# Kernel tuning notes

Measured on AMD Instinct MI355X. Metric: run time of the kernel, lower is better.

## Reference

```python
import jax, jax.numpy as jnp
import numpy as np
import math

L = 6; D = 768; NH = 12; DH = D // NH; V = 2048; CTX = 512; B = 16; T = 512
PAD_ID = 0; PAD_X = 18; PAD_Y = 32; N_ACTIONS = 9


def _layernorm(x, s, b, eps=1e-5):
    m = jnp.mean(x, axis=-1, keepdims=True)
    v = jnp.mean((x - m) ** 2, axis=-1, keepdims=True)
    return (x - m) * jax.lax.rsqrt(v + eps) * s + b


def setup_inputs() -> dict:
    key = jax.random.key(0)
    ks = jax.random.split(key, 16)
    s = 0.02
    x_emb = jax.random.normal(ks[4], (19, D), jnp.float32) * s
    x_emb = x_emb.at[PAD_X].set(0.0)  # padding_idx row is zero in torch
    y_emb = jax.random.normal(ks[5], (33, D), jnp.float32) * s
    y_emb = y_emb.at[PAD_Y].set(0.0)
    return {
        "history_cards": jax.random.randint(ks[0], (B, T), 0, V),
        "history_players": jax.random.randint(ks[1], (B, T), 0, 2),
        "deck": jax.random.randint(ks[2], (B, 8), 0, V),
        "opp_deck": jax.random.randint(ks[3], (B, 8), 0, V),
        "tok_emb": jax.random.normal(ks[6], (V, D), jnp.float32) * s,
        "player_emb": jax.random.normal(ks[7], (2, D), jnp.float32) * s,
        "pos_emb": jax.random.normal(ks[8], (CTX, D), jnp.float32) * s,
        "x_emb": x_emb,
        "y_emb": y_emb,
        "ln1_s": jnp.ones((L, D), jnp.float32),
        "ln1_b": jnp.zeros((L, D), jnp.float32),
        "qkv_w": jax.random.normal(ks[9], (L, D, 3 * D), jnp.float32) * s,
        "qkv_b": jnp.zeros((L, 3 * D), jnp.float32),
        "proj_w": jax.random.normal(ks[10], (L, D, D), jnp.float32) * s,
        "proj_b": jnp.zeros((L, D), jnp.float32),
        "ln2_s": jnp.ones((L, D), jnp.float32),
        "ln2_b": jnp.zeros((L, D), jnp.float32),
        "fc1_w": jax.random.normal(ks[11], (L, D, 4 * D), jnp.float32) * s,
        "fc1_b": jnp.zeros((L, 4 * D), jnp.float32),
        "fc2_w": jax.random.normal(ks[12], (L, 4 * D, D), jnp.float32) * s,
        "fc2_b": jnp.zeros((L, D), jnp.float32),
        "lnf_s": jnp.ones((D,), jnp.float32),
        "lnf_b": jnp.zeros((D,), jnp.float32),
        "head_w": jax.random.normal(ks[13], (D, N_ACTIONS), jnp.float32) * s,
        "head_b": jnp.zeros((N_ACTIONS,), jnp.float32),
    }


def reference(history_cards, history_players, deck, opp_deck,
              tok_emb, player_emb, pos_emb, x_emb, y_emb,
              ln1_s, ln1_b, qkv_w, qkv_b, proj_w, proj_b,
              ln2_s, ln2_b, fc1_w, fc1_b, fc2_w, fc2_b,
              lnf_s, lnf_b, head_w, head_b):
    Bc, Tc = history_cards.shape
    attn_mask = history_cards != PAD_ID                      # (B,T) True = valid
    all_pad = ~jnp.any(attn_mask, axis=1)
    attn_mask = attn_mask.at[:, 0].set(attn_mask[:, 0] | all_pad)

    # multi-embedding sum (history_x/history_y are None => padding rows = 0)
    h = (tok_emb[history_cards]
         + player_emb[jnp.clip(history_players, 0, 1)]
         + x_emb[PAD_X] + y_emb[PAD_Y]
         + jnp.mean(tok_emb[deck], axis=1, keepdims=True)
         + jnp.mean(tok_emb[opp_deck], axis=1, keepdims=True))
    x = h + pos_emb[:Tc][None]                               # (B,T,D)

    causal = jnp.tril(jnp.ones((Tc, Tc), bool))
    mask = causal[None, None, :, :] & attn_mask[:, None, None, :]  # (B,1,T,T)
    neg_inf = jnp.float32(-jnp.inf)
    scale = 1.0 / math.sqrt(DH)

    for i in range(L):
        # attention
        xn = _layernorm(x, ln1_s[i], ln1_b[i])
        qkv = xn @ qkv_w[i] + qkv_b[i]
        q, k, v = jnp.split(qkv, 3, axis=-1)
        q = q.reshape(Bc, Tc, NH, DH)
        k = k.reshape(Bc, Tc, NH, DH)
        v = v.reshape(Bc, Tc, NH, DH)
        scores = jnp.einsum('bihd,bjhd->bhij', q, k) * scale
        scores = jnp.where(mask, scores, neg_inf)
        w = jax.nn.softmax(scores, axis=-1)
        w = jnp.nan_to_num(w, nan=0.0, posinf=0.0, neginf=0.0)
        y = jnp.einsum('bhij,bjhd->bihd', w, v).reshape(Bc, Tc, D)
        x = x + (y @ proj_w[i] + proj_b[i])
        # MLP
        xn = _layernorm(x, ln2_s[i], ln2_b[i])
        hmid = jax.nn.gelu(xn @ fc1_w[i] + fc1_b[i], approximate=False)
        x = x + (hmid @ fc2_w[i] + fc2_b[i])

    x = _layernorm(x, lnf_s, lnf_b)
    last_idx = jnp.clip(jnp.sum(attn_mask.astype(jnp.int32), axis=1) - 1, 0, None)
    last_h = x[jnp.arange(Bc), last_idx]                     # (B,D)
    return last_h @ head_w + head_b                          # (B,9)
```

## Files before the change

### kernel.cpp

```cpp
#include <hip/hip_runtime.h>
#include <hip/hip_bf16.h>
#include <math.h>

typedef __hip_bfloat16 bf16;
typedef __bf16 bf16x8 __attribute__((ext_vector_type(8)));
typedef float f32x4 __attribute__((ext_vector_type(4)));

__device__ __forceinline__ float b2f(bf16 v){ return __bfloat162float(v); }
__device__ __forceinline__ bf16  f2b(float v){ return __float2bfloat16(v); }

__device__ __forceinline__ float gelu_f(float v){
    float y = v * (1.f + 0.044715f * v * v);
    return v / (1.f + __expf(-1.5957691216057308f * y));
}

__device__ __forceinline__ void gl_lds16(const bf16* g, bf16* l) {
    __builtin_amdgcn_global_load_lds((const __attribute__((address_space(1))) unsigned int*)g,
                                     (__attribute__((address_space(3))) unsigned int*)l, 16, 0, 0);
}

__device__ __forceinline__ uint2 pack4bf(const float* v){
    union { unsigned short e[4]; uint2 u; } pk;
    #pragma unroll
    for (int r = 0; r < 4; r++) pk.e[r] = __builtin_bit_cast(unsigned short, f2b(v[r]));
    return pk.u;
}

__device__ __forceinline__ void phase_bar() {
    __builtin_amdgcn_sched_barrier(0);
    __builtin_amdgcn_s_barrier();
    __builtin_amdgcn_sched_barrier(0);
}

__device__ __forceinline__ void supertile_map(int bid, int ntc, int& mt, int& nt) {
    const int slot = bid >> 3, xcd = bid & 7;
    const int g = 4 * ntc;
    const int chunk = slot / g;
    const int r = slot - chunk * g;
    const int ml = r / ntc;
    mt = xcd * 4 + ml;
    nt = chunk * ntc + (r - ml * ntc);
}

__global__ __launch_bounds__(256) void deckmean_k(const int* __restrict__ deck, const int* __restrict__ opp,
                                                  const float* __restrict__ tok, float* __restrict__ deckm)
{
    int b = blockIdx.x, w = blockIdx.y;
    const int* dk = (w ? opp : deck) + b * 8;
    int idx[8];
    #pragma unroll
    for (int j = 0; j < 8; j++) idx[j] = dk[j];
    float* out = deckm + (size_t)(w * 16 + b) * 768;
    for (int d = threadIdx.x; d < 768; d += 256) {
        float s = 0.f;
        #pragma unroll
        for (int j = 0; j < 8; j++) s += tok[(size_t)idx[j] * 768 + d];
        out[d] = s * 0.125f;
    }
}

__global__ __launch_bounds__(512) void mask_k(const int* __restrict__ cards, int* __restrict__ maskb,
                                              int* __restrict__ lastidx)
{
    int b = blockIdx.x, t = threadIdx.x;
    int m = (cards[b * 512 + t] != 0) ? 1 : 0;
    maskb[b * 512 + t] = m;
    __shared__ int red[512];
    red[t] = m; __syncthreads();
    for (int st = 256; st > 0; st >>= 1) { if (t < st) red[t] += red[t + st]; __syncthreads(); }
    if (t == 0) {
        int cnt = red[0];
        if (cnt == 0) { maskb[b * 512] = 1; cnt = 1; }
        lastidx[b] = cnt - 1;
    }
}

__global__ __launch_bounds__(256) void embed_k(const int* __restrict__ cards, const int* __restrict__ players,
                                               const float* __restrict__ tok, const float* __restrict__ pemb,
                                               const float* __restrict__ pos, const float* __restrict__ deckm,
                                               float* __restrict__ x)
{
    int t = blockIdx.x;
    int b = t >> 9, ti = t & 511;
    int cd = cards[t];
    int p = players[t]; p = p < 0 ? 0 : (p > 1 ? 1 : p);
    const float* tr  = tok  + (size_t)cd * 768;
    const float* pr  = pemb + (size_t)p  * 768;
    const float* po  = pos  + (size_t)ti * 768;
    const float* dm = deckm + (size_t)b * 768;
    const float* om = deckm + (size_t)(16 + b) * 768;
    float* xr = x + (size_t)t * 768;
    for (int d = threadIdx.x; d < 768; d += 256)
        xr[d] = tr[d] + pr[d] + po[d] + dm[d] + om[d];
}

__global__ __launch_bounds__(192) void ln_k(const float* __restrict__ x, const float* __restrict__ s,
                                            const float* __restrict__ b, bf16* __restrict__ out)
{
    int row = blockIdx.x, tid = threadIdx.x;
    float4 v = ((const float4*)(x + (size_t)row * 768))[tid];
    float sum = v.x + v.y + v.z + v.w;
    float sq  = v.x * v.x + v.y * v.y + v.z * v.z + v.w * v.w;
    #pragma unroll
    for (int off = 32; off > 0; off >>= 1) {
        sum += __shfl_xor(sum, off, 64);
        sq  += __shfl_xor(sq,  off, 64);
    }
    __shared__ float red[6];
    int wv = tid >> 6;
    if ((tid & 63) == 0) { red[wv] = sum; red[3 + wv] = sq; }
    __syncthreads();
    float S = red[0] + red[1] + red[2];
    float Q = red[3] + red[4] + red[5];
    float mean = S * (1.f / 768.f);
    float var  = Q * (1.f / 768.f) - mean * mean;
    float rstd = rsqrtf(var + 1e-5f);
    float4 sv = ((const float4*)s)[tid];
    float4 bv = ((const float4*)b)[tid];
    float o[4] = { (v.x - mean) * rstd * sv.x + bv.x, (v.y - mean) * rstd * sv.y + bv.y,
                   (v.z - mean) * rstd * sv.z + bv.z, (v.w - mean) * rstd * sv.w + bv.w };
    ((uint2*)(out + (size_t)row * 768))[tid] = pack4bf(o);
}

__global__ __launch_bounds__(256) void transpose4_k(const float* __restrict__ qw, const float* __restrict__ pw,
                                                    const float* __restrict__ f1, const float* __restrict__ f2,
                                                    bf16* __restrict__ oq, bf16* __restrict__ op,
                                                    bf16* __restrict__ o1, bf16* __restrict__ o2)
{
    int t = blockIdx.x;
    const float* in; bf16* out; int K, N, nbx;
    if (t < 432)       { in = qw; out = oq; K = 768;  N = 2304; nbx = 36; }
    else if (t < 576)  { in = pw; out = op; K = 768;  N = 768;  t -= 432;  nbx = 12; }
    else if (t < 1152) { in = f1; out = o1; K = 768;  N = 3072; t -= 576;  nbx = 48; }
    else               { in = f2; out = o2; K = 3072; N = 768;  t -= 1152; nbx = 12; }
    int n0 = (t % nbx) * 64, k0 = (t / nbx) * 64;
    int kq = threadIdx.x & 15, nq = threadIdx.x >> 4;
    float4 rr[4];
    #pragma unroll
    for (int r = 0; r < 4; r++)
        rr[r] = *(const float4*)&in[(size_t)(k0 + kq * 4 + r) * N + n0 + nq * 4];
    const float* fp = (const float*)rr;
    #pragma unroll
    for (int c = 0; c < 4; c++) {
        float v[4] = { fp[c], fp[4 + c], fp[8 + c], fp[12 + c] };
        *(uint2*)&out[(size_t)(n0 + nq * 4 + c) * K + k0 + kq * 4] = pack4bf(v);
    }
}

__global__ __launch_bounds__(512, 2) void gemmn128b_k(const bf16* __restrict__ A, const bf16* __restrict__ BT,
                                                      const float* __restrict__ bias, bf16* __restrict__ out,
                                                      int N, int K, int act, int ntc)
{
    __shared__ __align__(16) bf16 MA0[256 * 64];
    __shared__ __align__(16) bf16 MA1[256 * 64];
    __shared__ __align__(16) bf16 MA2[256 * 64];
    __shared__ __align__(16) bf16 MB0[128 * 64];
    __shared__ __align__(16) bf16 MB1[128 * 64];
    __shared__ __align__(16) bf16 MB2[128 * 64];

    const int tid  = threadIdx.x;
    const int lane = tid & 63, wid = tid >> 6;
    const int quad = lane >> 4, l16 = lane & 15;
    const int wr = wid >> 1, wc = wid & 1;
    const int cg0 = quad ^ (l16 & 7);
    const int cg1 = cg0 ^ 4;

    int mt, nt;
    supertile_map((int)blockIdx.x, ntc, mt, nt);
    const int m0 = mt * 256, n0 = nt * 128;

    const int srow = wid * 8 + (lane >> 3);
    const int scg  = (lane & 7) ^ (lane >> 3);
    const bf16* sa[4]; const bf16* sb[2];
    #pragma unroll
    for (int s = 0; s < 4; s++) sa[s] = A  + (size_t)(m0 + s * 64 + srow) * K + scg * 8;
    #pragma unroll
    for (int s = 0; s < 2; s++) sb[s] = BT + (size_t)(n0 + s * 64 + srow) * K + scg * 8;

#define MSTG6(NA, NB) { \
    gl_lds16(sa[0], &NA[(0 * 64 + wid * 8) * 64]); gl_lds16(sa[1], &NA[(1 * 64 + wid * 8) * 64]); \
    gl_lds16(sa[2], &NA[(2 * 64 + wid * 8) * 64]); gl_lds16(sa[3], &NA[(3 * 64 + wid * 8) * 64]); \
    gl_lds16(sb[0], &NB[(0 * 64 + wid * 8) * 64]); gl_lds16(sb[1], &NB[(1 * 64 + wid * 8) * 64]); }
#define MADV { _Pragma("unroll") for (int s = 0; s < 4; s++) sa[s] += 64; sb[0] += 64; sb[1] += 64; }
#define MLD(cg, NA, NB) { _Pragma("unroll") for (int i = 0; i < 4; i++) { \
    bfv[i] = __builtin_bit_cast(bf16x8, *(const uint4*)&NB[(wc * 64 + i * 16 + l16) * 64 + (cg) * 8]); \
    afv[i] = __builtin_bit_cast(bf16x8, *(const uint4*)&NA[(wr * 64 + i * 16 + l16) * 64 + (cg) * 8]); } }
#define MMFMA { _Pragma("unroll") for (int mi = 0; mi < 4; mi++) \
    _Pragma("unroll") for (int ni = 0; ni < 4; ni++) \
        acc[mi][ni] = __builtin_amdgcn_mfma_f32_16x16x32_bf16(bfv[ni], afv[mi], acc[mi][ni], 0, 0, 0); }
#define MITER(NAc, NBc, NAs, NBs) { \
    const bool pf = (kt + 2 < NKT); \
    MLD(cg0, NAc, NBc); \
    if (pf) { MSTG6(NAs, NBs); MADV; } \
    phase_bar(); \
    __builtin_amdgcn_s_setprio(1); MMFMA; __builtin_amdgcn_s_setprio(0); \
    phase_bar(); \
    MLD(cg1, NAc, NBc); \
    phase_bar(); \
    __builtin_amdgcn_s_setprio(1); MMFMA; __builtin_amdgcn_s_setprio(0); \
    if (pf)               { asm volatile("s_waitcnt vmcnt(6)" ::: "memory"); phase_bar(); } \
    else if (kt + 1 < NKT){ asm volatile("s_waitcnt vmcnt(0)" ::: "memory"); phase_bar(); } \
    kt++; \
}

    f32x4 acc[4][4] = {};
    const int NKT = K >> 6;

    MSTG6(MA0, MB0); MADV;
    MSTG6(MA1, MB1); MADV;
    asm volatile("s_waitcnt vmcnt(6)" ::: "memory");
    phase_bar();

    int kt = 0;
    bf16x8 bfv[4], afv[4];
    #pragma unroll 1
    for (int kt3 = 0; kt3 < NKT; kt3 += 3) {
        MITER(MA0, MB0, MA2, MB2);
        MITER(MA1, MB1, MA0, MB0);
        MITER(MA2, MB2, MA1, MB1);
    }

    float4 bv4[4];
    #pragma unroll
    for (int ni = 0; ni < 4; ni++)
        bv4[ni] = *(const float4*)&bias[n0 + wc * 64 + ni * 16 + quad * 4];

    #pragma unroll
    for (int mi = 0; mi < 4; mi++) {
        const int m = m0 + wr * 64 + mi * 16 + l16;
        #pragma unroll
        for (int ni = 0; ni < 4; ni++) {
            const int nb2 = n0 + wc * 64 + ni * 16 + quad * 4;
            float v[4] = { acc[mi][ni][0] + bv4[ni].x, acc[mi][ni][1] + bv4[ni].y,
                           acc[mi][ni][2] + bv4[ni].z, acc[mi][ni][3] + bv4[ni].w };
            if (act) {
                #pragma unroll
                for (int r = 0; r < 4; r++) v[r] = gelu_f(v[r]);
            }
            *(uint2*)&out[(size_t)m * N + nb2] = pack4bf(v);
        }
    }
#undef MSTG6
#undef MADV
#undef MLD
#undef MMFMA
#undef MITER
}

__global__ __launch_bounds__(512, 2) void gemmn128_k(const bf16* __restrict__ A, const bf16* __restrict__ BT,
                                                     const float* __restrict__ bias, float* __restrict__ x,
                                                     int N, int K, int ntc)
{
    __shared__ __align__(16) bf16 NA0[256 * 64];
    __shared__ __align__(16) bf16 NA1[256 * 64];
    __shared__ __align__(16) bf16 NA2[256 * 64];
    __shared__ __align__(16) bf16 NB0[128 * 64];
    __shared__ __align__(16) bf16 NB1[128 * 64];
    __shared__ __align__(16) bf16 NB2[128 * 64];

    const int tid  = threadIdx.x;
    const int lane = tid & 63, wid = tid >> 6;
    const int quad = lane >> 4, l16 = lane & 15;
    const int wr = wid >> 1, wc = wid & 1;
    const int cg0 = quad ^ (l16 & 7);
    const int cg1 = cg0 ^ 4;

    int mt, nt;
    supertile_map((int)blockIdx.x, ntc, mt, nt);
    const int m0 = mt * 256, n0 = nt * 128;

    const int srow = wid * 8 + (lane >> 3);
    const int scg  = (lane & 7) ^ (lane >> 3);
    const bf16* sa[4]; const bf16* sb[2];
    #pragma unroll
    for (int s = 0; s < 4; s++) sa[s] = A  + (size_t)(m0 + s * 64 + srow) * K + scg * 8;
    #pragma unroll
    for (int s = 0; s < 2; s++) sb[s] = BT + (size_t)(n0 + s * 64 + srow) * K + scg * 8;

#define NSTG6(NA, NB) { \
    gl_lds16(sa[0], &NA[(0 * 64 + wid * 8) * 64]); gl_lds16(sa[1], &NA[(1 * 64 + wid * 8) * 64]); \
    gl_lds16(sa[2], &NA[(2 * 64 + wid * 8) * 64]); gl_lds16(sa[3], &NA[(3 * 64 + wid * 8) * 64]); \
    gl_lds16(sb[0], &NB[(0 * 64 + wid * 8) * 64]); gl_lds16(sb[1], &NB[(1 * 64 + wid * 8) * 64]); }
#define NADV { _Pragma("unroll") for (int s = 0; s < 4; s++) sa[s] += 64; sb[0] += 64; sb[1] += 64; }
#define NLD(cg, NA, NB) { _Pragma("unroll") for (int i = 0; i < 4; i++) { \
    bfv[i] = __builtin_bit_cast(bf16x8, *(const uint4*)&NB[(wc * 64 + i * 16 + l16) * 64 + (cg) * 8]); \
    afv[i] = __builtin_bit_cast(bf16x8, *(const uint4*)&NA[(wr * 64 + i * 16 + l16) * 64 + (cg) * 8]); } }
#define NMFMA { _Pragma("unroll") for (int mi = 0; mi < 4; mi++) \
    _Pragma("unroll") for (int ni = 0; ni < 4; ni++) \
        acc[mi][ni] = __builtin_amdgcn_mfma_f32_16x16x32_bf16(bfv[ni], afv[mi], acc[mi][ni], 0, 0, 0); }
#define NITER(NAc, NBc, NAs, NBs) { \
    const bool pf = (kt + 2 < NKT); \
    NLD(cg0, NAc, NBc); \
    if (pf) { NSTG6(NAs, NBs); NADV; } \
    phase_bar(); \
    __builtin_amdgcn_s_setprio(1); NMFMA; __builtin_amdgcn_s_setprio(0); \
    phase_bar(); \
    NLD(cg1, NAc, NBc); \
    phase_bar(); \
    __builtin_amdgcn_s_setprio(1); NMFMA; __builtin_amdgcn_s_setprio(0); \
    if (pf)               { asm volatile("s_waitcnt vmcnt(6)" ::: "memory"); phase_bar(); } \
    else if (kt + 1 < NKT){ asm volatile("s_waitcnt vmcnt(0)" ::: "memory"); phase_bar(); } \
    kt++; \
}

    f32x4 acc[4][4] = {};
    const int NKT = K >> 6;

    NSTG6(NA0, NB0); NADV;
    NSTG6(NA1, NB1); NADV;
    asm volatile("s_waitcnt vmcnt(6)" ::: "memory");
    phase_bar();

    int kt = 0;
    bf16x8 bfv[4], afv[4];
    #pragma unroll 1
    for (int kt3 = 0; kt3 < NKT; kt3 += 3) {
        NITER(NA0, NB0, NA2, NB2);
        NITER(NA1, NB1, NA0, NB0);
        NITER(NA2, NB2, NA1, NB1);
    }

    float4 bv4[4];
    #pragma unroll
    for (int ni = 0; ni < 4; ni++)
        bv4[ni] = *(const float4*)&bias[n0 + wc * 64 + ni * 16 + quad * 4];

    #pragma unroll
    for (int mi = 0; mi < 4; mi++) {
        const int m = m0 + wr * 64 + mi * 16 + l16;
        #pragma unroll
        for (int ni = 0; ni < 4; ni++) {
            const int nb2 = n0 + wc * 64 + ni * 16 + quad * 4;
            float* xp = &x[(size_t)m * N + nb2];
            float4 xo = *(float4*)xp;
            xo.x += acc[mi][ni][0] + bv4[ni].x;
            xo.y += acc[mi][ni][1] + bv4[ni].y;
            xo.z += acc[mi][ni][2] + bv4[ni].z;
            xo.w += acc[mi][ni][3] + bv4[ni].w;
            *(float4*)xp = xo;
        }
    }
#undef NSTG6
#undef NADV
#undef NLD
#undef NMFMA
#undef NITER
}

__global__ __launch_bounds__(256) void attn_k(const bf16* __restrict__ qkv, const int* __restrict__ mask,
                                              bf16* __restrict__ y)
{
    const int qt = blockIdx.x, h = blockIdx.y, b = blockIdx.z;
    const int qbase = qt * 128, tokb = b * 512;
    __shared__ __align__(16) unsigned short Kl[128][72];
    __shared__ __align__(16) unsigned short Vt[64][136];
    __shared__ __align__(16) unsigned short Ptq[4][16][136];
    __shared__ float mkf[128];

    const int tid = threadIdx.x, wave = tid >> 6, lane = tid & 63;
    const int quad = lane >> 4, l16 = lane & 15;

    bf16x8 bq[2][2];
    #pragma unroll
    for (int qc = 0; qc < 2; qc++) {
        const bf16* qp = &qkv[(size_t)(tokb + qbase + wave * 32 + qc * 16 + l16) * 2304 + h * 64];
        bq[qc][0] = __builtin_bit_cast(bf16x8, *(const uint4*)(qp + quad * 8));
        bq[qc][1] = __builtin_bit_cast(bf16x8, *(const uint4*)(qp + 32 + quad * 8));
    }

    float m_i[2] = { -INFINITY, -INFINITY }, l_i[2] = { 0.f, 0.f };
    f32x4 Oacc[2][4] = {};

    const int nst = qt + 1;
    for (int s = 0; s < nst; s++) {
        const int j0 = s * 128;
        __syncthreads();
        {
            int key = tid >> 1, c0 = (tid & 1) * 32;
            const bf16* kg = &qkv[(size_t)(tokb + j0 + key) * 2304 + 768  + h * 64 + c0];
            const bf16* vg = &qkv[(size_t)(tokb + j0 + key) * 2304 + 1536 + h * 64 + c0];
            #pragma unroll
            for (int q = 0; q < 4; q++)
                *(uint4*)&Kl[key][c0 + q * 8] = *(const uint4*)(kg + q * 8);
            union { uint4 u[4]; unsigned short e[32]; } vv;
            #pragma unroll
            for (int q = 0; q < 4; q++) vv.u[q] = *(const uint4*)(vg + q * 8);
            #pragma unroll
            for (int j = 0; j < 32; j++) Vt[c0 + j][key] = vv.e[j];
            if (tid < 128) mkf[tid] = mask[b * 512 + j0 + tid] ? 0.f : -INFINITY;
        }
        __syncthreads();

        #pragma unroll
        for (int qc = 0; qc < 2; qc++) {
            const int qi = qbase + wave * 32 + qc * 16 + l16;

            f32x4 sc[8] = {};
            #pragma unroll
            for (int kcc = 0; kcc < 8; kcc++) {
                bf16x8 af0 = __builtin_bit_cast(bf16x8, *(const uint4*)&Kl[kcc * 16 + l16][quad * 8]);
                bf16x8 af1 = __builtin_bit_cast(bf16x8, *(const uint4*)&Kl[kcc * 16 + l16][32 + quad * 8]);
                sc[kcc] = __builtin_amdgcn_mfma_f32_16x16x32_bf16(af0, bq[qc][0], sc[kcc], 0, 0, 0);
                sc[kcc] = __builtin_amdgcn_mfma_f32_16x16x32_bf16(af1, bq[qc][1], sc[kcc], 0, 0, 0);
            }

            float pv[8][4];
            float mx = -INFINITY;
            #pragma unroll
            for (int kcc = 0; kcc < 8; kcc++) {
                float4 mk4 = *(const float4*)&mkf[kcc * 16 + quad * 4];
                float mkr[4] = { mk4.x, mk4.y, mk4.z, mk4.w };
                #pragma unroll
                for (int r = 0; r < 4; r++) {
                    int krel = kcc * 16 + quad * 4 + r;
                    float sval = (j0 + krel <= qi) ? (sc[kcc][r] * 0.125f + mkr[r]) : -INFINITY;
                    pv[kcc][r] = sval;
                    mx = fmaxf(mx, sval);
                }
            }
            mx = fmaxf(mx, __shfl_xor(mx, 16, 64));
            mx = fmaxf(mx, __shfl_xor(mx, 32, 64));
            float mn = fmaxf(m_i[qc], mx);
            float alpha = (mn == -INFINITY) ? 1.f : __expf(m_i[qc] - mn);
            float lsum = 0.f;
            #pragma unroll
            for (int kcc = 0; kcc < 8; kcc++)
                #pragma unroll
                for (int r = 0; r < 4; r++) {
                    float pp = (pv[kcc][r] == -INFINITY) ? 0.f : __expf(pv[kcc][r] - mn);
                    pv[kcc][r] = pp; lsum += pp;
                }
            lsum += __shfl_xor(lsum, 16, 64);
            lsum += __shfl_xor(lsum, 32, 64);
            m_i[qc] = mn; l_i[qc] = alpha * l_i[qc] + lsum;

            #pragma unroll
            for (int kcc = 0; kcc < 8; kcc++)
                *(uint2*)&Ptq[wave][l16][kcc * 16 + quad * 4] = pack4bf(pv[kcc]);
            #pragma unroll
            for (int mc = 0; mc < 4; mc++)
                #pragma unroll
                for (int r = 0; r < 4; r++) Oacc[qc][mc][r] *= alpha;

            __syncthreads();

            #pragma unroll
            for (int kcc = 0; kcc < 4; kcc++) {
                bf16x8 pb = __builtin_bit_cast(bf16x8, *(const uint4*)&Ptq[wave][l16][kcc * 32 + quad * 8]);
                #pragma unroll
                for (int mc = 0; mc < 4; mc++) {
                    bf16x8 vf = __builtin_bit_cast(bf16x8, *(const uint4*)&Vt[mc * 16 + l16][kcc * 32 + quad * 8]);
                    Oacc[qc][mc] = __builtin_amdgcn_mfma_f32_16x16x32_bf16(vf, pb, Oacc[qc][mc], 0, 0, 0);
                }
            }
        }
    }

    #pragma unroll
    for (int qc = 0; qc < 2; qc++) {
        float inv = (l_i[qc] > 0.f) ? 1.f / l_i[qc] : 0.f;
        const int tok = tokb + qbase + wave * 32 + qc * 16 + l16;
        #pragma unroll
        for (int mc = 0; mc < 4; mc++) {
            float v[4] = { Oacc[qc][mc][0] * inv, Oacc[qc][mc][1] * inv,
                           Oacc[qc][mc][2] * inv, Oacc[qc][mc][3] * inv };
            *(uint2*)&y[(size_t)tok * 768 + h * 64 + mc * 16 + quad * 4] = pack4bf(v);
        }
    }
}

__global__ __launch_bounds__(256) void head_k(const float* __restrict__ x, const int* __restrict__ lastidx,
                                              const float* __restrict__ ls, const float* __restrict__ lb,
                                              const float* __restrict__ hw, const float* __restrict__ hb,
                                              float* __restrict__ out)
{
    int b = blockIdx.x, tid = threadIdx.x;
    const float* xr = x + ((size_t)(b * 512 + lastidx[b])) * 768;
    float v0 = xr[tid], v1 = xr[tid + 256], v2 = xr[tid + 512];
    __shared__ float rs[256], rq[256];
    rs[tid] = v0 + v1 + v2; rq[tid] = v0 * v0 + v1 * v1 + v2 * v2;
    __syncthreads();
    for (int st = 128; st > 0; st >>= 1) {
        if (tid < st) { rs[tid] += rs[tid + st]; rq[tid] += rq[tid + st]; }
        __syncthreads();
    }
    float mean = rs[0] * (1.f / 768.f);
    float var  = rq[0] * (1.f / 768.f) - mean * mean;
    float rstd = rsqrtf(var + 1e-5f);
    float part[9];
    #pragma unroll
    for (int a = 0; a < 9; a++) part[a] = 0.f;
    float vv[3] = { v0, v1, v2 };
    #pragma unroll
    for (int e = 0; e < 3; e++) {
        int d = tid + e * 256;
        float xnv = (vv[e] - mean) * rstd * ls[d] + lb[d];
        #pragma unroll
        for (int a = 0; a < 9; a++) part[a] += xnv * hw[d * 9 + a];
    }
    __shared__ float r9[9][256];
    #pragma unroll
    for (int a = 0; a < 9; a++) r9[a][tid] = part[a];
    __syncthreads();
    for (int st = 128; st > 0; st >>= 1) {
        if (tid < st) {
            for (int a = 0; a < 9; a++) r9[a][tid] += r9[a][tid + st];
        }
        __syncthreads();
    }
    if (tid < 9) out[b * 9 + tid] = r9[tid][0] + hb[tid];
}

extern "C" void kernel_launch(void* const* d_in, const int* in_sizes, int n_in,
                              void* d_out, int out_size, void* d_ws, size_t ws_size,
                              hipStream_t stream) {
    const int*   cards   = (const int*)  d_in[0];
    const int*   players = (const int*)  d_in[1];
    const int*   deck    = (const int*)  d_in[2];
    const int*   oppd    = (const int*)  d_in[3];
    const float* tok     = (const float*)d_in[4];
    const float* pemb    = (const float*)d_in[5];
    const float* pos     = (const float*)d_in[6];
    const float* ln1s  = (const float*)d_in[9];
    const float* ln1b  = (const float*)d_in[10];
    const float* qkvw  = (const float*)d_in[11];
    const float* qkvb  = (const float*)d_in[12];
    const float* projw = (const float*)d_in[13];
    const float* projb = (const float*)d_in[14];
    const float* ln2s  = (const float*)d_in[15];
    const float* ln2b  = (const float*)d_in[16];
    const float* fc1w  = (const float*)d_in[17];
    const float* fc1b  = (const float*)d_in[18];
    const float* fc2w  = (const float*)d_in[19];
    const float* fc2b  = (const float*)d_in[20];
    const float* lnfs  = (const float*)d_in[21];
    const float* lnfb  = (const float*)d_in[22];
    const float* hw    = (const float*)d_in[23];
    const float* hb    = (const float*)d_in[24];
    float* out = (float*)d_out;

    char* p = (char*)d_ws;
    auto alloc = [&](size_t bytes) { char* q = p; p += (bytes + 255) & ~((size_t)255); return q; };
    float* x     = (float*)alloc(8192ull * 768 * 4);
    bf16*  xn    = (bf16*) alloc(8192ull * 768 * 2);
    bf16*  big   = (bf16*) alloc(8192ull * 3072 * 2);
    bf16*  wt    = (bf16*) alloc(7077888ull * 2);
    float* deckm = (float*)alloc(2ull * 16 * 768 * 4);
    int*   maskb = (int*)  alloc(8192ull * 4);
    int*   lasti = (int*)  alloc(64);

    bf16* wq = wt;
    bf16* wp = wq + 2304ull * 768;
    bf16* w1 = wp + 768ull * 768;
    bf16* w2 = w1 + 3072ull * 768;

    deckmean_k<<<dim3(16, 2), 256, 0, stream>>>(deck, oppd, tok, deckm);
    mask_k<<<16, 512, 0, stream>>>(cards, maskb, lasti);
    embed_k<<<8192, 256, 0, stream>>>(cards, players, tok, pemb, pos, deckm, x);

    for (int i = 0; i < 6; i++) {
        transpose4_k<<<1728, 256, 0, stream>>>(
            qkvw + (size_t)i * 768 * 2304, projw + (size_t)i * 768 * 768,
            fc1w + (size_t)i * 768 * 3072, fc2w + (size_t)i * 3072 * 768,
            wq, wp, w1, w2);

        ln_k<<<8192, 192, 0, stream>>>(x, ln1s + i * 768, ln1b + i * 768, xn);
        gemmn128b_k<<<576, 512, 0, stream>>>(xn, wq, qkvb + i * 2304, big, 2304, 768, 0, 6);
        attn_k<<<dim3(4, 12, 16), 256, 0, stream>>>(big, maskb, xn);
        gemmn128_k<<<192, 512, 0, stream>>>(xn, wp, projb + i * 768, x, 768, 768, 6);
        ln_k<<<8192, 192, 0, stream>>>(x, ln2s + i * 768, ln2b + i * 768, xn);
        gemmn128b_k<<<768, 512, 0, stream>>>(xn, w1, fc1b + i * 3072, big, 3072, 768, 1, 8);
        gemmn128_k<<<192, 512, 0, stream>>>(big, w2, fc2b + i * 768, x, 768, 3072, 6);
    }

    head_k<<<16, 256, 0, stream>>>(x, lasti, lnfs, lnfb, hw, hb, out);
}
```

Before: 1.787 ms.

## Replace 256x128 triple-buffered QKV/FC1 GEMM with 128x128 double-buffered 4-wave kernel

The QKV and FC1 GEMMs switch from a 512-thread kernel with 256x128 tiles and three-stage LDS buffering to a 256-thread kernel with 128x128 tiles and two-stage buffering. A new supertile mapping with eight row-tiles per XCD goes with it, and the launches grow to 1152 and 1536 blocks. The aim is to raise block count and occupancy and to simplify the per-tile barrier schedule, with one barrier per k-tile instead of several. In exchange, each tile reuses less data per global load, and the loop waits with vmcnt(0) every iteration, so prefetch overlap is shallower.

```diff
diff --git a/kernel.cpp b/kernel.cpp
--- a/kernel.cpp
+++ b/kernel.cpp
@@ -39,6 +39,16 @@
     const int r = slot - chunk * g;
     const int ml = r / ntc;
     mt = xcd * 4 + ml;
+    nt = chunk * ntc + (r - ml * ntc);
+}
+
+__device__ __forceinline__ void supertile_map8(int bid, int ntc, int& mt, int& nt) {
+    const int slot = bid >> 3, xcd = bid & 7;
+    const int g = 8 * ntc;
+    const int chunk = slot / g;
+    const int r = slot - chunk * g;
+    const int ml = r / ntc;
+    mt = xcd * 8 + ml;
     nt = chunk * ntc + (r - ml * ntc);
 }
 
@@ -147,16 +157,14 @@
     }
 }
 
-__global__ __launch_bounds__(512, 2) void gemmn128b_k(const bf16* __restrict__ A, const bf16* __restrict__ BT,
-                                                      const float* __restrict__ bias, bf16* __restrict__ out,
-                                                      int N, int K, int act, int ntc)
-{
-    __shared__ __align__(16) bf16 MA0[256 * 64];
-    __shared__ __align__(16) bf16 MA1[256 * 64];
-    __shared__ __align__(16) bf16 MA2[256 * 64];
-    __shared__ __align__(16) bf16 MB0[128 * 64];
-    __shared__ __align__(16) bf16 MB1[128 * 64];
-    __shared__ __align__(16) bf16 MB2[128 * 64];
+__global__ __launch_bounds__(256, 2) void gemm2b_k(const bf16* __restrict__ A, const bf16* __restrict__ BT,
+                                                   const float* __restrict__ bias, bf16* __restrict__ out,
+                                                   int N, int K, int act, int ntc)
+{
+    __shared__ __align__(16) bf16 DA0[128 * 64];
+    __shared__ __align__(16) bf16 DA1[128 * 64];
+    __shared__ __align__(16) bf16 DB0[128 * 64];
+    __shared__ __align__(16) bf16 DB1[128 * 64];
 
     const int tid  = threadIdx.x;
     const int lane = tid & 63, wid = tid >> 6;
@@ -166,58 +174,55 @@
     const int cg1 = cg0 ^ 4;
 
     int mt, nt;
-    supertile_map((int)blockIdx.x, ntc, mt, nt);
-    const int m0 = mt * 256, n0 = nt * 128;
+    supertile_map8((int)blockIdx.x, ntc, mt, nt);
+    const int m0 = mt * 128, n0 = nt * 128;
 
     const int srow = wid * 8 + (lane >> 3);
     const int scg  = (lane & 7) ^ (lane >> 3);
-    const bf16* sa[4]; const bf16* sb[2];
-    #pragma unroll
-    for (int s = 0; s < 4; s++) sa[s] = A  + (size_t)(m0 + s * 64 + srow) * K + scg * 8;
-    #pragma unroll
-    for (int s = 0; s < 2; s++) sb[s] = BT + (size_t)(n0 + s * 64 + srow) * K + scg * 8;
-
-#define MSTG6(NA, NB) { \
-    gl_lds16(sa[0], &NA[(0 * 64 + wid * 8) * 64]); gl_lds16(sa[1], &NA[(1 * 64 + wid * 8) * 64]); \
-    gl_lds16(sa[2], &NA[(2 * 64 + wid * 8) * 64]); gl_lds16(sa[3], &NA[(3 * 64 + wid * 8) * 64]); \
-    gl_lds16(sb[0], &NB[(0 * 64 + wid * 8) * 64]); gl_lds16(sb[1], &NB[(1 * 64 + wid * 8) * 64]); }
-#define MADV { _Pragma("unroll") for (int s = 0; s < 4; s++) sa[s] += 64; sb[0] += 64; sb[1] += 64; }
-#define MLD(cg, NA, NB) { _Pragma("unroll") for (int i = 0; i < 4; i++) { \
+    const bf16* sa[4]; const bf16* sb[4];
+    #pragma unroll
+    for (int s = 0; s < 4; s++) {
+        sa[s] = A  + (size_t)(m0 + s * 32 + srow) * K + scg * 8;
+        sb[s] = BT + (size_t)(n0 + s * 32 + srow) * K + scg * 8;
+    }
+
+#define D_STG8(NA, NB) { \
+    gl_lds16(sa[0], &NA[(0 * 32 + wid * 8) * 64]); gl_lds16(sa[1], &NA[(1 * 32 + wid * 8) * 64]); \
+    gl_lds16(sa[2], &NA[(2 * 32 + wid * 8) * 64]); gl_lds16(sa[3], &NA[(3 * 32 + wid * 8) * 64]); \
+    gl_lds16(sb[0], &NB[(0 * 32 + wid * 8) * 64]); gl_lds16(sb[1], &NB[(1 * 32 + wid * 8) * 64]); \
+    gl_lds16(sb[2], &NB[(2 * 32 + wid * 8) * 64]); gl_lds16(sb[3], &NB[(3 * 32 + wid * 8) * 64]); }
+#define D_ADV { _Pragma("unroll") for (int s = 0; s < 4; s++) { sa[s] += 64; sb[s] += 64; } }
+#define D_LD(cg, NA, NB) { _Pragma("unroll") for (int i = 0; i < 4; i++) { \
     bfv[i] = __builtin_bit_cast(bf16x8, *(const uint4*)&NB[(wc * 64 + i * 16 + l16) * 64 + (cg) * 8]); \
     afv[i] = __builtin_bit_cast(bf16x8, *(const uint4*)&NA[(wr * 64 + i * 16 + l16) * 64 + (cg) * 8]); } }
-#define MMFMA { _Pragma("unroll") for (int mi = 0; mi < 4; mi++) \
+#define D_MFMA { _Pragma("unroll") for (int mi = 0; mi < 4; mi++) \
     _Pragma("unroll") for (int ni = 0; ni < 4; ni++) \
         acc[mi][ni] = __builtin_amdgcn_mfma_f32_16x16x32_bf16(bfv[ni], afv[mi], acc[mi][ni], 0, 0, 0); }
-#define MITER(NAc, NBc, NAs, NBs) { \
-    const bool pf = (kt + 2 < NKT); \
-    MLD(cg0, NAc, NBc); \
-    if (pf) { MSTG6(NAs, NBs); MADV; } \
+#define D_TILE(DAc, DBc, DAn, DBn) { \
+    const bool pf = (kt + 1 < NKT); \
+    D_LD(cg0, DAc, DBc); \
+    if (pf) { D_STG8(DAn, DBn); D_ADV; } \
+    __builtin_amdgcn_s_setprio(1); D_MFMA; __builtin_amdgcn_s_setprio(0); \
+    D_LD(cg1, DAc, DBc); \
+    __builtin_amdgcn_s_setprio(1); D_MFMA; __builtin_amdgcn_s_setprio(0); \
+    if (pf) { asm volatile("s_waitcnt vmcnt(0)" ::: "memory"); } \
     phase_bar(); \
-    __builtin_amdgcn_s_setprio(1); MMFMA; __builtin_amdgcn_s_setprio(0); \
-    phase_bar(); \
-    MLD(cg1, NAc, NBc); \
-    phase_bar(); \
-    __builtin_amdgcn_s_setprio(1); MMFMA; __builtin_amdgcn_s_setprio(0); \
-    if (pf)               { asm volatile("s_waitcnt vmcnt(6)" ::: "memory"); phase_bar(); } \
-    else if (kt + 1 < NKT){ asm volatile("s_waitcnt vmcnt(0)" ::: "memory"); phase_bar(); } \
     kt++; \
 }
 
     f32x4 acc[4][4] = {};
     const int NKT = K >> 6;
 
-    MSTG6(MA0, MB0); MADV;
-    MSTG6(MA1, MB1); MADV;
-    asm volatile("s_waitcnt vmcnt(6)" ::: "memory");
+    D_STG8(DA0, DB0); D_ADV;
+    asm volatile("s_waitcnt vmcnt(0)" ::: "memory");
     phase_bar();
 
     int kt = 0;
     bf16x8 bfv[4], afv[4];
     #pragma unroll 1
-    for (int kt3 = 0; kt3 < NKT; kt3 += 3) {
-        MITER(MA0, MB0, MA2, MB2);
-        MITER(MA1, MB1, MA0, MB0);
-        MITER(MA2, MB2, MA1, MB1);
+    for (int kt2 = 0; kt2 < NKT; kt2 += 2) {
+        D_TILE(DA0, DB0, DA1, DB1);
+        D_TILE(DA1, DB1, DA0, DB0);
     }
 
     float4 bv4[4];
@@ -240,11 +245,11 @@
             *(uint2*)&out[(size_t)m * N + nb2] = pack4bf(v);
         }
     }
-#undef MSTG6
-#undef MADV
-#undef MLD
-#undef MMFMA
-#undef MITER
+#undef D_STG8
+#undef D_ADV
+#undef D_LD
+#undef D_MFMA
+#undef D_TILE
 }
 
 __global__ __launch_bounds__(512, 2) void gemmn128_k(const bf16* __restrict__ A, const bf16* __restrict__ BT,
@@ -565,11 +570,11 @@
             wq, wp, w1, w2);
 
         ln_k<<<8192, 192, 0, stream>>>(x, ln1s + i * 768, ln1b + i * 768, xn);
-        gemmn128b_k<<<576, 512, 0, stream>>>(xn, wq, qkvb + i * 2304, big, 2304, 768, 0, 6);
+        gemm2b_k<<<1152, 256, 0, stream>>>(xn, wq, qkvb + i * 2304, big, 2304, 768, 0, 6);
         attn_k<<<dim3(4, 12, 16), 256, 0, stream>>>(big, maskb, xn);
         gemmn128_k<<<192, 512, 0, stream>>>(xn, wp, projb + i * 768, x, 768, 768, 6);
         ln_k<<<8192, 192, 0, stream>>>(x, ln2s + i * 768, ln2b + i * 768, xn);
-        gemmn128b_k<<<768, 512, 0, stream>>>(xn, w1, fc1b + i * 3072, big, 3072, 768, 1, 8);
+        gemm2b_k<<<1536, 256, 0, stream>>>(xn, w1, fc1b + i * 3072, big, 3072, 768, 1, 8);
         gemmn128_k<<<192, 512, 0, stream>>>(big, w2, fc2b + i * 768, x, 768, 3072, 6);
     }
 
```

New measurement: 1.675 ms. -6.3%, faster.
